# Kernel tuning notes

Hardware: AMD Instinct MI355X
Metric: run time of the kernel (lower is better)

Reference implementation:

```python
import jax, jax.numpy as jnp
import numpy as np
from jax import lax

WSIZE = 11
SIGMA = 1.5
PAD = WSIZE // 2  # 5
C1 = 0.01 ** 2
C2 = 0.03 ** 2


def _gauss1d():
    x = np.arange(WSIZE) - WSIZE // 2
    g = np.exp(-(x.astype(np.float64) ** 2) / (2.0 * SIGMA ** 2))
    g = g / g.sum()
    return jnp.asarray(g, dtype=jnp.float32)


def _blur3d(x, g):
    """Replicate-pad by 5 on D/H/W then apply the separable 11x11x11 Gaussian.
    x: [N, 1, D, H, W]. Mathematically identical to the dense conv3d in the
    original (the 3D window is an exact outer product of the 1D Gaussian)."""
    xp = jnp.pad(x, ((0, 0), (0, 0), (PAD, PAD), (PAD, PAD), (PAD, PAD)), mode='edge')
    dn = ('NCDHW', 'OIDHW', 'NCDHW')
    for kshape in ((1, 1, WSIZE, 1, 1), (1, 1, 1, WSIZE, 1), (1, 1, 1, 1, WSIZE)):
        xp = lax.conv_general_dilated(xp, g.reshape(kshape), (1, 1, 1), 'VALID',
                                      dimension_numbers=dn)
    return xp


def _rerange(img):
    img = jnp.where(img.max() > 128.0, img / 255.0, img)
    img = jnp.where(img.min() < -0.5, (img + 1.0) / 2.0, img)
    return img


def setup_inputs() -> dict:
    key = jax.random.key(0)
    k1, k2 = jax.random.split(key)
    N, C, H, W = 4, 16, 512, 512
    pred = jax.random.uniform(k1, (N, C, H, W), dtype=jnp.float32)
    gt = jax.random.uniform(k2, (N, C, H, W), dtype=jnp.float32)
    return {"pred": pred, "gt": gt}


def reference(pred, gt):
    N = pred.shape[0]
    pred = _rerange(pred)
    gt = _rerange(gt)

    # ---- PSNR (range = 1.0, reduce='sum') ----
    mse = jnp.mean((pred - gt) ** 2, axis=(1, 2, 3))           # [N]
    psnr = jnp.sum(10.0 * jnp.log10(1.0 / mse))                # scalar

    # ---- 3D SSIM over [N,1,C,H,W] volumes ----
    g = _gauss1d()
    img = pred[:, None]                                        # [N,1,D,H,W]
    gtt = gt[:, None]
    mu1 = _blur3d(img, g)
    mu2 = _blur3d(gtt, g)
    mu1_sq = mu1 * mu1
    mu2_sq = mu2 * mu2
    mu1_mu2 = mu1 * mu2
    sigma1_sq = _blur3d(img * img, g) - mu1_sq
    sigma2_sq = _blur3d(gtt * gtt, g) - mu2_sq
    sigma12 = _blur3d(img * gtt, g) - mu1_mu2

    v1 = 2.0 * sigma12 + C2
    v2 = sigma1_sq + sigma2_sq + C2
    ssim_map = ((2.0 * mu1_mu2 + C1) * v1) / ((mu1_sq + mu2_sq + C1) * v2)
    ssim = jnp.sum(jnp.mean(ssim_map, axis=(1, 2, 3, 4)))      # reduce='sum'

    return psnr, ssim, N
```

## Files before the change

### kernel.cpp

```cpp
#include <hip/hip_runtime.h>
#include <cmath>


#define NB 4
#define DD 16
#define HH 512
#define WW 512
#define SLICE (HH * WW)
#define VOL (DD * SLICE)
#define C1F 0.0001f
#define C2F 0.0009f

#define TH 16
#define TW 16
#define SCOLS 26
#define NRP 13
#define PW 14
#define PLSTR 28
#define SDW (NRP * PLSTR)
#define TMW (TH * PW)
#define NTHR 256
#define SIT (NRP * SCOLS)
#define XTRA (SIT - NTHR)
#define HITEMS 104

typedef _Float16 h2v __attribute__((ext_vector_type(2)));

struct KArg {
  unsigned ge[6], go[6];
  float wlT[DD * DD];
};

__device__ inline float dot2h(unsigned a, unsigned b, float c) {
#if __has_builtin(__builtin_amdgcn_fdot2)
  return __builtin_amdgcn_fdot2(__builtin_bit_cast(h2v, a),
                                __builtin_bit_cast(h2v, b), c, false);
#else
  h2v av = __builtin_bit_cast(h2v, a), bv = __builtin_bit_cast(h2v, b);
  return fmaf((float)av.y, (float)bv.y, fmaf((float)av.x, (float)bv.x, c));
#endif
}
__device__ inline unsigned pkh(float a, float b) {
  return __builtin_bit_cast(unsigned, __builtin_amdgcn_cvt_pkrtz(a, b));
}
__device__ inline int iclamp(int v, int lo, int hi) {
  return v < lo ? lo : (v > hi ? hi : v);
}

__device__ inline float block_sum256(float v) {
#pragma unroll
  for (int o = 32; o > 0; o >>= 1) v += __shfl_down(v, o, 64);
  __shared__ float r[4];
  if ((threadIdx.x & 63) == 0) r[threadIdx.x >> 6] = v;
  __syncthreads();
  float out = 0.f;
  if (threadIdx.x == 0) {
#pragma unroll
    for (int i = 0; i < 4; ++i) out += r[i];
  }
  __syncthreads();
  return out;
}

__global__ void zero_acc_k(float* acc) {
  if (threadIdx.x < 8) acc[threadIdx.x] = 0.f;
}

__global__ __launch_bounds__(NTHR, 3) void fused_k(
    const float* __restrict__ pred, const float* __restrict__ gt,
    float* __restrict__ acc, KArg ka) {
  __shared__ uint4 sd[SDW];
  __shared__ uint4 tmp[TMW];

  int b = blockIdx.x;
  int tile = b & 1023;
  int n = b >> 10;
  int th0 = (tile >> 5) * TH;
  int tw0 = (tile & 31) * TW;
  int t = threadIdx.x;

  int rp0 = t / SCOLS, x0 = t - rp0 * SCOLS;
  int gx0 = iclamp(tw0 + x0 - 5, 0, WW - 1);
  int go0a = iclamp(th0 + 2 * rp0 - 5, 0, HH - 1) * WW + gx0;
  int go0b = iclamp(th0 + 2 * rp0 - 4, 0, HH - 1) * WW + gx0;
  int w0i = (2 * rp0 + (x0 & 1)) * PW + (x0 >> 1);
  bool ox0 = (x0 >= 5) && (x0 < 5 + TW);
  float o0a = (ox0 && rp0 >= 3 && rp0 <= 10) ? 1.f : 0.f;
  float o0b = (ox0 && rp0 >= 2 && rp0 <= 9) ? 1.f : 0.f;
  int i1 = t + XTRA;
  bool has2 = (i1 >= NTHR);
  int rp1 = i1 / SCOLS, x1 = i1 - rp1 * SCOLS;
  int gx1 = iclamp(tw0 + x1 - 5, 0, WW - 1);
  int go1a = iclamp(th0 + 2 * rp1 - 5, 0, HH - 1) * WW + gx1;
  int go1b = iclamp(th0 + 2 * rp1 - 4, 0, HH - 1) * WW + gx1;
  int w1i = (2 * rp1 + (x1 & 1)) * PW + (x1 >> 1);
  bool ox1 = (x1 >= 5) && (x1 < 5 + TW);
  float o1a = (ox1 && rp1 >= 3 && rp1 <= 10) ? 1.f : 0.f;
  float o1b = (ox1 && rp1 >= 2 && rp1 <= 9) ? 1.f : 0.f;

  bool hasH = (t < HITEMS);
  int hm = t & 7, hcp = t >> 3;
  int hrd = hm * PLSTR + hcp;
  int hwr = (2 * hm) * PW + hcp;

  int wx = t & 15;
  int wrd = (t >> 4) * PW + (wx >> 1);
  unsigned cw[6];
#pragma unroll
  for (int J = 0; J < 6; ++J) cw[J] = (wx & 1) ? ka.go[J] : ka.ge[J];

  const float* pb = pred + (size_t)n * VOL;
  const float* qb = gt + (size_t)n * VOL;

  float p0a = pb[go0a], p0b = pb[go0b], q0a = qb[go0a], q0b = qb[go0b];
  float p1a = 0.f, p1b = 0.f, q1a = 0.f, q1b = 0.f;
  if (has2) { p1a = pb[go1a]; p1b = pb[go1b]; q1a = qb[go1a]; q1b = qb[go1b]; }

  float psnr = 0.f;
  float a0[DD], a1[DD], a2[DD], a3[DD];
#pragma unroll
  for (int j = 0; j < DD; ++j) { a0[j] = a1[j] = a2[j] = a3[j] = 0.f; }

#pragma unroll 1
  for (int d = 0; d < DD; ++d) {
    {
      float SA = p0a + q0a, DA = p0a - q0a;
      float SB = p0b + q0b, DB = p0b - q0b;
      float dA = DA * DA, dB = DB * DB;
      psnr = fmaf(o0a, dA, psnr);
      psnr = fmaf(o0b, dB, psnr);
      sd[w0i] = make_uint4(pkh(SA, SB), pkh(DA, DB),
                           pkh(SA * SA, SB * SB), pkh(dA, dB));
    }
    if (has2) {
      float SA = p1a + q1a, DA = p1a - q1a;
      float SB = p1b + q1b, DB = p1b - q1b;
      float dA = DA * DA, dB = DB * DB;
      psnr = fmaf(o1a, dA, psnr);
      psnr = fmaf(o1b, dB, psnr);
      sd[w1i] = make_uint4(pkh(SA, SB), pkh(DA, DB),
                           pkh(SA * SA, SB * SB), pkh(dA, dB));
    }
    __syncthreads();

    if (d < DD - 1) {
      const float* P = pb + (size_t)(d + 1) * SLICE;
      const float* Q = qb + (size_t)(d + 1) * SLICE;
      p0a = P[go0a]; p0b = P[go0b]; q0a = Q[go0a]; q0b = Q[go0b];
      if (has2) { p1a = P[go1a]; p1b = P[go1b]; q1a = Q[go1a]; q1b = Q[go1b]; }
    }

    if (hasH) {
      float e0[4] = {0, 0, 0, 0}, e1[4] = {0, 0, 0, 0};
      float r0[4] = {0, 0, 0, 0}, r1[4] = {0, 0, 0, 0};
#pragma unroll
      for (int J = 0; J < 6; ++J) {
        uint4 ve = sd[hrd + J * PLSTR];
        uint4 vo = sd[hrd + J * PLSTR + PW];
        unsigned cge = ka.ge[J], cgo = ka.go[J];
        e0[0] = dot2h(cge, ve.x, e0[0]); e0[1] = dot2h(cge, ve.y, e0[1]);
        e0[2] = dot2h(cge, ve.z, e0[2]); e0[3] = dot2h(cge, ve.w, e0[3]);
        r0[0] = dot2h(cgo, ve.x, r0[0]); r0[1] = dot2h(cgo, ve.y, r0[1]);
        r0[2] = dot2h(cgo, ve.z, r0[2]); r0[3] = dot2h(cgo, ve.w, r0[3]);
        e1[0] = dot2h(cge, vo.x, e1[0]); e1[1] = dot2h(cge, vo.y, e1[1]);
        e1[2] = dot2h(cge, vo.z, e1[2]); e1[3] = dot2h(cge, vo.w, e1[3]);
        r1[0] = dot2h(cgo, vo.x, r1[0]); r1[1] = dot2h(cgo, vo.y, r1[1]);
        r1[2] = dot2h(cgo, vo.z, r1[2]); r1[3] = dot2h(cgo, vo.w, r1[3]);
      }
      tmp[hwr] = make_uint4(pkh(e0[0], e1[0]), pkh(e0[1], e1[1]),
                            pkh(e0[2], e1[2]), pkh(e0[3], e1[3]));
      tmp[hwr + PW] = make_uint4(pkh(r0[0], r1[0]), pkh(r0[1], r1[1]),
                                 pkh(r0[2], r1[2]), pkh(r0[3], r1[3]));
    }
    __syncthreads();

    float w0 = 0.f, w1 = 0.f, w2 = 0.f, w3 = 0.f;
#pragma unroll
    for (int J = 0; J < 6; ++J) {
      uint4 v = tmp[wrd + J];
      w0 = dot2h(cw[J], v.x, w0); w1 = dot2h(cw[J], v.y, w1);
      w2 = dot2h(cw[J], v.z, w2); w3 = dot2h(cw[J], v.w, w3);
    }
    const float* wl = ka.wlT + d * DD;
#pragma unroll
    for (int o = 0; o < DD; ++o) {
      float w = wl[o];
      a0[o] = fmaf(w, w0, a0[o]);
      a1[o] = fmaf(w, w1, a1[o]);
      a2[o] = fmaf(w, w2, a2[o]);
      a3[o] = fmaf(w, w3, a3[o]);
    }
  }

  float ssum = 0.f;
#pragma unroll
  for (int j = 0; j < DD; ++j) {
    float Sb = a0[j], Db = a1[j], B1 = a2[j], B2 = a3[j];
    float SS = Sb * Sb, DDm = Db * Db;
    float m12_2 = (SS - DDm) * 0.5f;
    float msq   = (SS + DDm) * 0.5f;
    float Epq   = (B1 - B2) * 0.25f;
    float Esum  = (B1 + B2) * 0.5f;
    float sig12_2 = 2.f * Epq - m12_2;
    float svar    = Esum - msq;
    float num = (m12_2 + C1F) * (sig12_2 + C2F);
    float den = (msq + C1F) * (svar + C2F);
    ssum += num / den;
  }
  float bs = block_sum256(ssum);
  if (t == 0) atomicAdd(&acc[4 + n], bs);
  float bp = block_sum256(psnr);
  if (t == 0) atomicAdd(&acc[n], bp);
}

__global__ void final_k(const float* __restrict__ acc, float* __restrict__ out) {
  if (threadIdx.x == 0 && blockIdx.x == 0) {
    double psnr = 0.0, ssim = 0.0;
    for (int n = 0; n < NB; ++n) {
      double mse = (double)acc[n] / (double)VOL;
      psnr += 10.0 * log10(1.0 / mse);
      ssim += (double)acc[4 + n] / (double)VOL;
    }
    out[0] = (float)psnr;
    out[1] = (float)ssim;
    out[2] = (float)NB;
  }
}

static unsigned short f2h(float f) {
  union { float f; unsigned u; } v; v.f = f;
  unsigned u = v.u;
  unsigned s = (u >> 16) & 0x8000u;
  int e = (int)((u >> 23) & 0xff) - 127 + 15;
  unsigned m = u & 0x7fffffu;
  if (e <= 0) return (unsigned short)s;
  if (e >= 31) return (unsigned short)(s | 0x7c00u);
  unsigned h = ((unsigned)e << 10) | (m >> 13);
  unsigned rem = m & 0x1fffu;
  if (rem > 0x1000u || (rem == 0x1000u && (h & 1u))) h++;
  return (unsigned short)(s | h);
}
static float h2f(unsigned short h) {
  unsigned se = (h >> 10) & 0x1f, m = h & 0x3ffu, s = ((unsigned)h & 0x8000u) << 16;
  union { unsigned u; float f; } v;
  if (se == 0) { v.u = s; return v.f; }
  v.u = s | ((se - 15 + 127) << 23) | (m << 13);
  return v.f;
}

extern "C" void kernel_launch(void* const* d_in, const int* in_sizes, int n_in,
                              void* d_out, int out_size, void* d_ws, size_t ws_size,
                              hipStream_t stream) {
  const float* pred = (const float*)d_in[0];
  const float* gt = (const float*)d_in[1];
  float* acc = (float*)d_ws;

  double tt[11], s = 0.0;
  for (int i = 0; i < 11; ++i) {
    double x = i - 5;
    tt[i] = exp(-(x * x) / 4.5);
    s += tt[i];
  }
  float g[11];
  for (int i = 0; i < 11; ++i) g[i] = (float)(tt[i] / s);

  unsigned short hg[11];
  for (int i = 0; i < 11; ++i) hg[i] = f2h(g[i]);
  for (int pass = 0; pass < 3; ++pass) {
    double sum = 0.0;
    for (int i = 0; i < 11; ++i) sum += (double)h2f(hg[i]);
    hg[5] = f2h((float)((double)h2f(hg[5]) + (1.0 - sum)));
  }

  KArg ka;
  for (int j = 0; j < 5; ++j)
    ka.ge[j] = (unsigned)hg[2 * j] | ((unsigned)hg[2 * j + 1] << 16);
  ka.ge[5] = (unsigned)hg[10];
  ka.go[0] = ((unsigned)hg[0]) << 16;
  for (int j = 1; j < 6; ++j)
    ka.go[j] = (unsigned)hg[2 * j - 1] | ((unsigned)hg[2 * j] << 16);

  for (int o = 0; o < DD; ++o)
    for (int d = 0; d < DD; ++d) {
      float w = 0.f;
      for (int k = 0; k < 11; ++k) {
        int j = o + k - 5;
        j = j < 0 ? 0 : (j > 15 ? 15 : j);
        if (j == d) w += g[k];
      }
      ka.wlT[d * DD + o] = w;
    }

  zero_acc_k<<<1, 64, 0, stream>>>(acc);
  fused_k<<<NB * 1024, NTHR, 0, stream>>>(pred, gt, acc, ka);
  final_k<<<1, 1, 0, stream>>>(acc, (float*)d_out);
}
```

Baseline: 255.6 us.

## Replace dot2 separable blur passes with MFMA 16x16x32 f16 matrix products

Recasts the H, W and depth Gaussian passes as banded-matrix multiplies on MFMA f16 instructions, using lane-specific band tables uploaded to device memory instead of a kernel-argument struct. Depth accumulation now stores per-slice fp16 results to a larger LDS buffer and applies the clamped depth weights with MFMA at the end, instead of keeping 64 float accumulators in registers. The aim is to move the convolution arithmetic onto matrix cores and free registers. In exchange it uses more LDS, adds an extra barrier per slice, rounds intermediates to fp16 more often, and issues a host-to-device copy of the tables on every call.

Result: slower. 295.2 us (+15.5%).

```diff
diff --git a/kernel.cpp b/kernel.cpp
--- a/kernel.cpp
+++ b/kernel.cpp
@@ -13,32 +13,14 @@
 
 #define TH 16
 #define TW 16
-#define SCOLS 26
-#define NRP 13
-#define PW 14
-#define PLSTR 28
-#define SDW (NRP * PLSTR)
-#define TMW (TH * PW)
 #define NTHR 256
-#define SIT (NRP * SCOLS)
-#define XTRA (SIT - NTHR)
-#define HITEMS 104
-
-typedef _Float16 h2v __attribute__((ext_vector_type(2)));
-
-struct KArg {
-  unsigned ge[6], go[6];
-  float wlT[DD * DD];
-};
-
-__device__ inline float dot2h(unsigned a, unsigned b, float c) {
-#if __has_builtin(__builtin_amdgcn_fdot2)
-  return __builtin_amdgcn_fdot2(__builtin_bit_cast(h2v, a),
-                                __builtin_bit_cast(h2v, b), c, false);
-#else
-  h2v av = __builtin_bit_cast(h2v, a), bv = __builtin_bit_cast(h2v, b);
-  return fmaf((float)av.y, (float)bv.y, fmaf((float)av.x, (float)bv.x, c));
-#endif
+
+typedef _Float16 h8 __attribute__((ext_vector_type(8)));
+typedef float f4 __attribute__((ext_vector_type(4)));
+
+__device__ inline f4 mfma16(uint4 a, uint4 b, f4 c) {
+  return __builtin_amdgcn_mfma_f32_16x16x32_f16(
+      __builtin_bit_cast(h8, a), __builtin_bit_cast(h8, b), c, 0, 0, 0);
 }
 __device__ inline unsigned pkh(float a, float b) {
   return __builtin_bit_cast(unsigned, __builtin_amdgcn_cvt_pkrtz(a, b));
@@ -68,9 +50,10 @@
 
 __global__ __launch_bounds__(NTHR, 3) void fused_k(
     const float* __restrict__ pred, const float* __restrict__ gt,
-    float* __restrict__ acc, KArg ka) {
-  __shared__ uint4 sd[SDW];
-  __shared__ uint4 tmp[TMW];
+    float* __restrict__ acc, const uint4* __restrict__ tabs) {
+  __shared__ _Float16 sd[4 * 32 * 40];
+  __shared__ _Float16 ost[4 * 256 * 16];
+  __shared__ uint4 zzq;
 
   int b = blockIdx.x;
   int tile = b & 1023;
@@ -78,36 +61,36 @@
   int th0 = (tile >> 5) * TH;
   int tw0 = (tile & 31) * TW;
   int t = threadIdx.x;
-
-  int rp0 = t / SCOLS, x0 = t - rp0 * SCOLS;
+  int lane = t & 63, wv = t >> 6;
+  int lo = lane & 15, hi = lane >> 4;
+
+  uint4 bh = tabs[lane];
+  uint4 gwt = tabs[64 + lane];
+  uint4 wlf = tabs[128 + lane];
+
+  unsigned* sdw = (unsigned*)sd;
+#pragma unroll
+  for (int i = 0; i < 10; ++i) sdw[t + i * 256] = 0;
+  if (t == 0) zzq = make_uint4(0, 0, 0, 0);
+
+  int rp0 = t / 26, x0 = t - rp0 * 26;
   int gx0 = iclamp(tw0 + x0 - 5, 0, WW - 1);
   int go0a = iclamp(th0 + 2 * rp0 - 5, 0, HH - 1) * WW + gx0;
   int go0b = iclamp(th0 + 2 * rp0 - 4, 0, HH - 1) * WW + gx0;
-  int w0i = (2 * rp0 + (x0 & 1)) * PW + (x0 >> 1);
-  bool ox0 = (x0 >= 5) && (x0 < 5 + TW);
+  int w0 = x0 * 20 + rp0;
+  bool ox0 = (x0 >= 5) && (x0 < 21);
   float o0a = (ox0 && rp0 >= 3 && rp0 <= 10) ? 1.f : 0.f;
   float o0b = (ox0 && rp0 >= 2 && rp0 <= 9) ? 1.f : 0.f;
-  int i1 = t + XTRA;
-  bool has2 = (i1 >= NTHR);
-  int rp1 = i1 / SCOLS, x1 = i1 - rp1 * SCOLS;
+  int i1 = t + 82;
+  bool has2 = (i1 >= 256);
+  int rp1 = i1 / 26, x1 = i1 - rp1 * 26;
   int gx1 = iclamp(tw0 + x1 - 5, 0, WW - 1);
   int go1a = iclamp(th0 + 2 * rp1 - 5, 0, HH - 1) * WW + gx1;
   int go1b = iclamp(th0 + 2 * rp1 - 4, 0, HH - 1) * WW + gx1;
-  int w1i = (2 * rp1 + (x1 & 1)) * PW + (x1 >> 1);
-  bool ox1 = (x1 >= 5) && (x1 < 5 + TW);
+  int w1 = x1 * 20 + rp1;
+  bool ox1 = (x1 >= 5) && (x1 < 21);
   float o1a = (ox1 && rp1 >= 3 && rp1 <= 10) ? 1.f : 0.f;
   float o1b = (ox1 && rp1 >= 2 && rp1 <= 9) ? 1.f : 0.f;
-
-  bool hasH = (t < HITEMS);
-  int hm = t & 7, hcp = t >> 3;
-  int hrd = hm * PLSTR + hcp;
-  int hwr = (2 * hm) * PW + hcp;
-
-  int wx = t & 15;
-  int wrd = (t >> 4) * PW + (wx >> 1);
-  unsigned cw[6];
-#pragma unroll
-  for (int J = 0; J < 6; ++J) cw[J] = (wx & 1) ? ka.go[J] : ka.ge[J];
 
   const float* pb = pred + (size_t)n * VOL;
   const float* qb = gt + (size_t)n * VOL;
@@ -116,10 +99,20 @@
   float p1a = 0.f, p1b = 0.f, q1a = 0.f, q1b = 0.f;
   if (has2) { p1a = pb[go1a]; p1b = pb[go1b]; q1a = qb[go1a]; q1b = qb[go1b]; }
 
+  int owb = wv * 1024 + (64 * hi + lo) * 4;
+  int qx = 2 * (hi & 1);
+  const uint4* sdq = (const uint4*)sd;
+  int fr0 = wv * 160 + lo * 5 + hi;
+  int fr1 = wv * 160 + (lo + 16) * 5 + hi;
+  f4 z4 = {0.f, 0.f, 0.f, 0.f};
+
   float psnr = 0.f;
-  float a0[DD], a1[DD], a2[DD], a3[DD];
-#pragma unroll
-  for (int j = 0; j < DD; ++j) { a0[j] = a1[j] = a2[j] = a3[j] = 0.f; }
+  float oe0, oe1, oe2, oe3;
+  unsigned pA0, pA1, pA2, pA3, pB0, pB1, pB2, pB3;
+  oe0 = oe1 = oe2 = oe3 = 0.f;
+  pA0 = pA1 = pA2 = pA3 = pB0 = pB1 = pB2 = pB3 = 0u;
+
+  __syncthreads();
 
 #pragma unroll 1
   for (int d = 0; d < DD; ++d) {
@@ -129,8 +122,10 @@
       float dA = DA * DA, dB = DB * DB;
       psnr = fmaf(o0a, dA, psnr);
       psnr = fmaf(o0b, dB, psnr);
-      sd[w0i] = make_uint4(pkh(SA, SB), pkh(DA, DB),
-                           pkh(SA * SA, SB * SB), pkh(dA, dB));
+      sdw[w0]        = pkh(SA, SB);
+      sdw[640 + w0]  = pkh(DA, DB);
+      sdw[1280 + w0] = pkh(SA * SA, SB * SB);
+      sdw[1920 + w0] = pkh(dA, dB);
     }
     if (has2) {
       float SA = p1a + q1a, DA = p1a - q1a;
@@ -138,9 +133,15 @@
       float dA = DA * DA, dB = DB * DB;
       psnr = fmaf(o1a, dA, psnr);
       psnr = fmaf(o1b, dB, psnr);
-      sd[w1i] = make_uint4(pkh(SA, SB), pkh(DA, DB),
-                           pkh(SA * SA, SB * SB), pkh(dA, dB));
-    }
+      sdw[w1]        = pkh(SA, SB);
+      sdw[640 + w1]  = pkh(DA, DB);
+      sdw[1280 + w1] = pkh(SA * SA, SB * SB);
+      sdw[1920 + w1] = pkh(dA, dB);
+    }
+    __syncthreads();
+
+    uint4 fa0 = sdq[fr0];
+    uint4 fa1 = sdq[fr1];
     __syncthreads();
 
     if (d < DD - 1) {
@@ -150,62 +151,61 @@
       if (has2) { p1a = P[go1a]; p1b = P[go1b]; q1a = Q[go1a]; q1b = Q[go1b]; }
     }
 
-    if (hasH) {
-      float e0[4] = {0, 0, 0, 0}, e1[4] = {0, 0, 0, 0};
-      float r0[4] = {0, 0, 0, 0}, r1[4] = {0, 0, 0, 0};
-#pragma unroll
-      for (int J = 0; J < 6; ++J) {
-        uint4 ve = sd[hrd + J * PLSTR];
-        uint4 vo = sd[hrd + J * PLSTR + PW];
-        unsigned cge = ka.ge[J], cgo = ka.go[J];
-        e0[0] = dot2h(cge, ve.x, e0[0]); e0[1] = dot2h(cge, ve.y, e0[1]);
-        e0[2] = dot2h(cge, ve.z, e0[2]); e0[3] = dot2h(cge, ve.w, e0[3]);
-        r0[0] = dot2h(cgo, ve.x, r0[0]); r0[1] = dot2h(cgo, ve.y, r0[1]);
-        r0[2] = dot2h(cgo, ve.z, r0[2]); r0[3] = dot2h(cgo, ve.w, r0[3]);
-        e1[0] = dot2h(cge, vo.x, e1[0]); e1[1] = dot2h(cge, vo.y, e1[1]);
-        e1[2] = dot2h(cge, vo.z, e1[2]); e1[3] = dot2h(cge, vo.w, e1[3]);
-        r1[0] = dot2h(cgo, vo.x, r1[0]); r1[1] = dot2h(cgo, vo.y, r1[1]);
-        r1[2] = dot2h(cgo, vo.z, r1[2]); r1[3] = dot2h(cgo, vo.w, r1[3]);
-      }
-      tmp[hwr] = make_uint4(pkh(e0[0], e1[0]), pkh(e0[1], e1[1]),
-                            pkh(e0[2], e1[2]), pkh(e0[3], e1[3]));
-      tmp[hwr + PW] = make_uint4(pkh(r0[0], r1[0]), pkh(r0[1], r1[1]),
-                                 pkh(r0[2], r1[2]), pkh(r0[3], r1[3]));
-    }
-    __syncthreads();
-
-    float w0 = 0.f, w1 = 0.f, w2 = 0.f, w3 = 0.f;
-#pragma unroll
-    for (int J = 0; J < 6; ++J) {
-      uint4 v = tmp[wrd + J];
-      w0 = dot2h(cw[J], v.x, w0); w1 = dot2h(cw[J], v.y, w1);
-      w2 = dot2h(cw[J], v.z, w2); w3 = dot2h(cw[J], v.w, w3);
-    }
-    const float* wl = ka.wlT + d * DD;
-#pragma unroll
-    for (int o = 0; o < DD; ++o) {
-      float w = wl[o];
-      a0[o] = fmaf(w, w0, a0[o]);
-      a1[o] = fmaf(w, w1, a1[o]);
-      a2[o] = fmaf(w, w2, a2[o]);
-      a3[o] = fmaf(w, w3, a3[o]);
-    }
-  }
-
+    f4 t0 = mfma16(fa0, bh, z4);
+    f4 t1 = mfma16(fa1, bh, z4);
+    uint4 ta = make_uint4(pkh(t0.x, t0.y), pkh(t0.z, t0.w),
+                          pkh(t1.x, t1.y), pkh(t1.z, t1.w));
+    f4 o = mfma16(ta, gwt, z4);
+
+    if ((d & 1) == 0) {
+      oe0 = o.x; oe1 = o.y; oe2 = o.z; oe3 = o.w;
+    } else if ((d & 2) == 0) {
+      pA0 = pkh(oe0, o.x); pA1 = pkh(oe1, o.y);
+      pA2 = pkh(oe2, o.z); pA3 = pkh(oe3, o.w);
+    } else {
+      pB0 = pkh(oe0, o.x); pB1 = pkh(oe1, o.y);
+      pB2 = pkh(oe2, o.z); pB3 = pkh(oe3, o.w);
+      int Qp = (d >> 2) ^ qx;
+      uint2* op = (uint2*)ost;
+      op[owb + Qp]       = make_uint2(pA0, pB0);
+      op[owb + 64 + Qp]  = make_uint2(pA1, pB1);
+      op[owb + 128 + Qp] = make_uint2(pA2, pB2);
+      op[owb + 192 + Qp] = make_uint2(pA3, pB3);
+    }
+  }
+  __syncthreads();
+
+  const uint4* oq = (const uint4*)ost;
+  int bnt = wv & 1;
+  int blk = (hi < 2) ? (hi ^ bnt) : 0;
+  bool real = (hi < 2);
   float ssum = 0.f;
 #pragma unroll
-  for (int j = 0; j < DD; ++j) {
-    float Sb = a0[j], Db = a1[j], B1 = a2[j], B2 = a3[j];
-    float SS = Sb * Sb, DDm = Db * Db;
-    float m12_2 = (SS - DDm) * 0.5f;
-    float msq   = (SS + DDm) * 0.5f;
-    float Epq   = (B1 - B2) * 0.25f;
-    float Esum  = (B1 + B2) * 0.5f;
-    float sig12_2 = 2.f * Epq - m12_2;
-    float svar    = Esum - msq;
-    float num = (m12_2 + C1F) * (sig12_2 + C2F);
-    float den = (msq + C1F) * (svar + C2F);
-    ssum += num / den;
+  for (int q = 0; q < 4; ++q) {
+    int nt = 4 * wv + q;
+    int bidx = (16 * nt + lo) * 2 + blk;
+    const uint4* bp0 = real ? &oq[bidx] : &zzq;
+    const uint4* bp1 = real ? &oq[512 + bidx] : &zzq;
+    const uint4* bp2 = real ? &oq[1024 + bidx] : &zzq;
+    const uint4* bp3 = real ? &oq[1536 + bidx] : &zzq;
+    f4 cS = mfma16(wlf, *bp0, z4);
+    f4 cD = mfma16(wlf, *bp1, z4);
+    f4 cS2 = mfma16(wlf, *bp2, z4);
+    f4 cD2 = mfma16(wlf, *bp3, z4);
+#pragma unroll
+    for (int r = 0; r < 4; ++r) {
+      float Sb = cS[r], Db = cD[r], B1 = cS2[r], B2 = cD2[r];
+      float SS = Sb * Sb, DDm = Db * Db;
+      float m12_2 = (SS - DDm) * 0.5f;
+      float msq = (SS + DDm) * 0.5f;
+      float Epq = (B1 - B2) * 0.25f;
+      float Esum = (B1 + B2) * 0.5f;
+      float sig12_2 = 2.f * Epq - m12_2;
+      float svar = Esum - msq;
+      float num = (m12_2 + C1F) * (sig12_2 + C2F);
+      float den = (msq + C1F) * (svar + C2F);
+      ssum += num / den;
+    }
   }
   float bs = block_sum256(ssum);
   if (t == 0) atomicAdd(&acc[4 + n], bs);
@@ -248,6 +248,9 @@
   return v.f;
 }
 
+static unsigned s_tabs[192 * 4];
+static bool s_init = false;
+
 extern "C" void kernel_launch(void* const* d_in, const int* in_sizes, int n_in,
                               void* d_out, int out_size, void* d_ws, size_t ws_size,
                               hipStream_t stream) {
@@ -255,43 +258,74 @@
   const float* gt = (const float*)d_in[1];
   float* acc = (float*)d_ws;
 
-  double tt[11], s = 0.0;
-  for (int i = 0; i < 11; ++i) {
-    double x = i - 5;
-    tt[i] = exp(-(x * x) / 4.5);
-    s += tt[i];
-  }
-  float g[11];
-  for (int i = 0; i < 11; ++i) g[i] = (float)(tt[i] / s);
-
-  unsigned short hg[11];
-  for (int i = 0; i < 11; ++i) hg[i] = f2h(g[i]);
-  for (int pass = 0; pass < 3; ++pass) {
-    double sum = 0.0;
-    for (int i = 0; i < 11; ++i) sum += (double)h2f(hg[i]);
-    hg[5] = f2h((float)((double)h2f(hg[5]) + (1.0 - sum)));
-  }
-
-  KArg ka;
-  for (int j = 0; j < 5; ++j)
-    ka.ge[j] = (unsigned)hg[2 * j] | ((unsigned)hg[2 * j + 1] << 16);
-  ka.ge[5] = (unsigned)hg[10];
-  ka.go[0] = ((unsigned)hg[0]) << 16;
-  for (int j = 1; j < 6; ++j)
-    ka.go[j] = (unsigned)hg[2 * j - 1] | ((unsigned)hg[2 * j] << 16);
-
-  for (int o = 0; o < DD; ++o)
-    for (int d = 0; d < DD; ++d) {
-      float w = 0.f;
-      for (int k = 0; k < 11; ++k) {
-        int j = o + k - 5;
-        j = j < 0 ? 0 : (j > 15 ? 15 : j);
-        if (j == d) w += g[k];
-      }
-      ka.wlT[d * DD + o] = w;
-    }
-
+  if (!s_init) {
+    double tt[11], s = 0.0;
+    for (int i = 0; i < 11; ++i) {
+      double x = i - 5;
+      tt[i] = exp(-(x * x) / 4.5);
+      s += tt[i];
+    }
+    float g[11];
+    for (int i = 0; i < 11; ++i) g[i] = (float)(tt[i] / s);
+    unsigned short hg[11];
+    for (int i = 0; i < 11; ++i) hg[i] = f2h(g[i]);
+    for (int pass = 0; pass < 3; ++pass) {
+      double sum = 0.0;
+      for (int i = 0; i < 11; ++i) sum += (double)h2f(hg[i]);
+      hg[5] = f2h((float)((double)h2f(hg[5]) + (1.0 - sum)));
+    }
+    float wl[DD][DD];
+    for (int o = 0; o < DD; ++o)
+      for (int d = 0; d < DD; ++d) {
+        float w = 0.f;
+        for (int k = 0; k < 11; ++k) {
+          int j = o + k - 5;
+          j = j < 0 ? 0 : (j > 15 ? 15 : j);
+          if (j == d) w += g[k];
+        }
+        wl[d][o] = w;
+      }
+    unsigned short wlh[DD][DD];
+    for (int o = 0; o < DD; ++o) {
+      int dmx = 0;
+      for (int d = 0; d < DD; ++d) {
+        wlh[o][d] = f2h(wl[d][o]);
+        if (wl[d][o] > wl[dmx][o]) dmx = d;
+      }
+      for (int pass = 0; pass < 3; ++pass) {
+        double sum = 0.0;
+        for (int d = 0; d < DD; ++d) sum += (double)h2f(wlh[o][d]);
+        wlh[o][dmx] = f2h((float)((double)h2f(wlh[o][dmx]) + (1.0 - sum)));
+      }
+    }
+    for (int l = 0; l < 64; ++l) {
+      int lo = l & 15, hi = l >> 4;
+      unsigned short v[8];
+      for (int i = 0; i < 8; ++i) {
+        int idx = 8 * hi + i - lo;
+        v[i] = (idx >= 0 && idx <= 10) ? hg[idx] : 0;
+      }
+      for (int k = 0; k < 4; ++k)
+        s_tabs[l * 4 + k] = (unsigned)v[2 * k] | ((unsigned)v[2 * k + 1] << 16);
+      for (int i = 0; i < 8; ++i) {
+        int c = 4 * hi + (i & 3) + 16 * (i >> 2);
+        int idx = c - lo;
+        v[i] = (idx >= 0 && idx <= 10) ? hg[idx] : 0;
+      }
+      for (int k = 0; k < 4; ++k)
+        s_tabs[(64 + l) * 4 + k] = (unsigned)v[2 * k] | ((unsigned)v[2 * k + 1] << 16);
+      for (int i = 0; i < 8; ++i)
+        v[i] = (hi < 2) ? wlh[lo][8 * hi + i] : 0;
+      for (int k = 0; k < 4; ++k)
+        s_tabs[(128 + l) * 4 + k] = (unsigned)v[2 * k] | ((unsigned)v[2 * k + 1] << 16);
+    }
+    s_init = true;
+  }
+
+  hipMemcpyAsync((char*)d_ws + 64, s_tabs, sizeof(s_tabs),
+                 hipMemcpyHostToDevice, stream);
   zero_acc_k<<<1, 64, 0, stream>>>(acc);
-  fused_k<<<NB * 1024, NTHR, 0, stream>>>(pred, gt, acc, ka);
+  fused_k<<<NB * 1024, NTHR, 0, stream>>>(pred, gt, acc,
+                                          (const uint4*)((char*)d_ws + 64));
   final_k<<<1, 1, 0, stream>>>(acc, (float*)d_out);
 }
```

## Defer depth blur to packed fp16 dot products and raise occupancy

Applied to the files above, without the earlier changes.

Replaces the per-slice fp32 accumulation into 64 depth-output registers with storing each slice's blurred values as packed fp16 pairs (32 registers). The depth blur is then applied at the end using fdot2 with fp16-renormalized depth weights. It also fully unrolls the slice loop, raises launch bounds to 4 blocks per SIMD, and remaps block order to interleave batches across XCDs. This cuts register pressure and the FMAs per slice, at the cost of extra fp16 rounding in the depth stage.

Result: slower. 627.9 us (+145.7%).

```diff
diff --git a/kernel.cpp b/kernel.cpp
--- a/kernel.cpp
+++ b/kernel.cpp
@@ -28,7 +28,7 @@
 
 struct KArg {
   unsigned ge[6], go[6];
-  float wlT[DD * DD];
+  unsigned w2[128];
 };
 
 __device__ inline float dot2h(unsigned a, unsigned b, float c) {
@@ -66,13 +66,14 @@
   if (threadIdx.x < 8) acc[threadIdx.x] = 0.f;
 }
 
-__global__ __launch_bounds__(NTHR, 3) void fused_k(
+__global__ __launch_bounds__(NTHR, 4) void fused_k(
     const float* __restrict__ pred, const float* __restrict__ gt,
     float* __restrict__ acc, KArg ka) {
   __shared__ uint4 sd[SDW];
   __shared__ uint4 tmp[TMW];
 
-  int b = blockIdx.x;
+  int b0 = blockIdx.x;
+  int b = (b0 & 7) * ((NB * 1024) >> 3) + (b0 >> 3);
   int tile = b & 1023;
   int n = b >> 10;
   int th0 = (tile >> 5) * TH;
@@ -117,90 +118,96 @@
   if (has2) { p1a = pb[go1a]; p1b = pb[go1b]; q1a = qb[go1a]; q1b = qb[go1b]; }
 
   float psnr = 0.f;
-  float a0[DD], a1[DD], a2[DD], a3[DD];
-#pragma unroll
-  for (int j = 0; j < DD; ++j) { a0[j] = a1[j] = a2[j] = a3[j] = 0.f; }
-
-#pragma unroll 1
-  for (int d = 0; d < DD; ++d) {
-    {
-      float SA = p0a + q0a, DA = p0a - q0a;
-      float SB = p0b + q0b, DB = p0b - q0b;
-      float dA = DA * DA, dB = DB * DB;
-      psnr = fmaf(o0a, dA, psnr);
-      psnr = fmaf(o0b, dB, psnr);
-      sd[w0i] = make_uint4(pkh(SA, SB), pkh(DA, DB),
-                           pkh(SA * SA, SB * SB), pkh(dA, dB));
-    }
-    if (has2) {
-      float SA = p1a + q1a, DA = p1a - q1a;
-      float SB = p1b + q1b, DB = p1b - q1b;
-      float dA = DA * DA, dB = DB * DB;
-      psnr = fmaf(o1a, dA, psnr);
-      psnr = fmaf(o1b, dB, psnr);
-      sd[w1i] = make_uint4(pkh(SA, SB), pkh(DA, DB),
-                           pkh(SA * SA, SB * SB), pkh(dA, dB));
-    }
-    __syncthreads();
-
-    if (d < DD - 1) {
-      const float* P = pb + (size_t)(d + 1) * SLICE;
-      const float* Q = qb + (size_t)(d + 1) * SLICE;
-      p0a = P[go0a]; p0b = P[go0b]; q0a = Q[go0a]; q0b = Q[go0b];
-      if (has2) { p1a = P[go1a]; p1b = P[go1b]; q1a = Q[go1a]; q1b = Q[go1b]; }
-    }
-
-    if (hasH) {
-      float e0[4] = {0, 0, 0, 0}, e1[4] = {0, 0, 0, 0};
-      float r0[4] = {0, 0, 0, 0}, r1[4] = {0, 0, 0, 0};
-#pragma unroll
-      for (int J = 0; J < 6; ++J) {
-        uint4 ve = sd[hrd + J * PLSTR];
-        uint4 vo = sd[hrd + J * PLSTR + PW];
-        unsigned cge = ka.ge[J], cgo = ka.go[J];
-        e0[0] = dot2h(cge, ve.x, e0[0]); e0[1] = dot2h(cge, ve.y, e0[1]);
-        e0[2] = dot2h(cge, ve.z, e0[2]); e0[3] = dot2h(cge, ve.w, e0[3]);
-        r0[0] = dot2h(cgo, ve.x, r0[0]); r0[1] = dot2h(cgo, ve.y, r0[1]);
-        r0[2] = dot2h(cgo, ve.z, r0[2]); r0[3] = dot2h(cgo, ve.w, r0[3]);
-        e1[0] = dot2h(cge, vo.x, e1[0]); e1[1] = dot2h(cge, vo.y, e1[1]);
-        e1[2] = dot2h(cge, vo.z, e1[2]); e1[3] = dot2h(cge, vo.w, e1[3]);
-        r1[0] = dot2h(cgo, vo.x, r1[0]); r1[1] = dot2h(cgo, vo.y, r1[1]);
-        r1[2] = dot2h(cgo, vo.z, r1[2]); r1[3] = dot2h(cgo, vo.w, r1[3]);
-      }
-      tmp[hwr] = make_uint4(pkh(e0[0], e1[0]), pkh(e0[1], e1[1]),
-                            pkh(e0[2], e1[2]), pkh(e0[3], e1[3]));
-      tmp[hwr + PW] = make_uint4(pkh(r0[0], r1[0]), pkh(r0[1], r1[1]),
-                                 pkh(r0[2], r1[2]), pkh(r0[3], r1[3]));
-    }
-    __syncthreads();
-
-    float w0 = 0.f, w1 = 0.f, w2 = 0.f, w3 = 0.f;
-#pragma unroll
-    for (int J = 0; J < 6; ++J) {
-      uint4 v = tmp[wrd + J];
-      w0 = dot2h(cw[J], v.x, w0); w1 = dot2h(cw[J], v.y, w1);
-      w2 = dot2h(cw[J], v.z, w2); w3 = dot2h(cw[J], v.w, w3);
-    }
-    const float* wl = ka.wlT + d * DD;
-#pragma unroll
-    for (int o = 0; o < DD; ++o) {
-      float w = wl[o];
-      a0[o] = fmaf(w, w0, a0[o]);
-      a1[o] = fmaf(w, w1, a1[o]);
-      a2[o] = fmaf(w, w2, a2[o]);
-      a3[o] = fmaf(w, w3, a3[o]);
-    }
-  }
+  unsigned h0[8], h1[8], h2[8], h3[8];
+
+#define DO_SLICE(D)                                                         \
+  {                                                                         \
+    float SA = p0a + q0a, DA = p0a - q0a;                                   \
+    float SB = p0b + q0b, DB = p0b - q0b;                                   \
+    float dA = DA * DA, dB = DB * DB;                                       \
+    psnr = fmaf(o0a, dA, psnr);                                             \
+    psnr = fmaf(o0b, dB, psnr);                                             \
+    sd[w0i] = make_uint4(pkh(SA, SB), pkh(DA, DB),                          \
+                         pkh(SA * SA, SB * SB), pkh(dA, dB));               \
+  }                                                                         \
+  if (has2) {                                                               \
+    float SA = p1a + q1a, DA = p1a - q1a;                                   \
+    float SB = p1b + q1b, DB = p1b - q1b;                                   \
+    float dA = DA * DA, dB = DB * DB;                                       \
+    psnr = fmaf(o1a, dA, psnr);                                             \
+    psnr = fmaf(o1b, dB, psnr);                                             \
+    sd[w1i] = make_uint4(pkh(SA, SB), pkh(DA, DB),                          \
+                         pkh(SA * SA, SB * SB), pkh(dA, dB));               \
+  }                                                                         \
+  __syncthreads();            \
+  if ((D) < DD - 1) {                                                       \
+    const float* P = pb + (size_t)((D) + 1) * SLICE;                        \
+    const float* Q = qb + (size_t)((D) + 1) * SLICE;                        \
+    p0a = P[go0a]; p0b = P[go0b]; q0a = Q[go0a]; q0b = Q[go0b];             \
+    if (has2) { p1a = P[go1a]; p1b = P[go1b]; q1a = Q[go1a]; q1b = Q[go1b]; } \
+  }                                                                         \
+  if (hasH) {                                                               \
+    float e0[4] = {0, 0, 0, 0}, e1[4] = {0, 0, 0, 0};                       \
+    float r0[4] = {0, 0, 0, 0}, r1[4] = {0, 0, 0, 0};                       \
+    _Pragma("unroll")                                                       \
+    for (int J = 0; J < 6; ++J) {                                           \
+      uint4 ve = sd[hrd + J * PLSTR];                                       \
+      uint4 vo = sd[hrd + J * PLSTR + PW];                                  \
+      unsigned cge = ka.ge[J], cgo = ka.go[J];                              \
+      e0[0] = dot2h(cge, ve.x, e0[0]); e0[1] = dot2h(cge, ve.y, e0[1]);     \
+      e0[2] = dot2h(cge, ve.z, e0[2]); e0[3] = dot2h(cge, ve.w, e0[3]);     \
+      r0[0] = dot2h(cgo, ve.x, r0[0]); r0[1] = dot2h(cgo, ve.y, r0[1]);     \
+      r0[2] = dot2h(cgo, ve.z, r0[2]); r0[3] = dot2h(cgo, ve.w, r0[3]);     \
+      e1[0] = dot2h(cge, vo.x, e1[0]); e1[1] = dot2h(cge, vo.y, e1[1]);     \
+      e1[2] = dot2h(cge, vo.z, e1[2]); e1[3] = dot2h(cge, vo.w, e1[3]);     \
+      r1[0] = dot2h(cgo, vo.x, r1[0]); r1[1] = dot2h(cgo, vo.y, r1[1]);     \
+      r1[2] = dot2h(cgo, vo.z, r1[2]); r1[3] = dot2h(cgo, vo.w, r1[3]);     \
+    }                                                                       \
+    tmp[hwr] = make_uint4(pkh(e0[0], e1[0]), pkh(e0[1], e1[1]),             \
+                          pkh(e0[2], e1[2]), pkh(e0[3], e1[3]));            \
+    tmp[hwr + PW] = make_uint4(pkh(r0[0], r1[0]), pkh(r0[1], r1[1]),        \
+                               pkh(r0[2], r1[2]), pkh(r0[3], r1[3]));       \
+  }                                                                         \
+  __syncthreads();   \
+  ww0 = 0.f; ww1 = 0.f; ww2 = 0.f; ww3 = 0.f;                               \
+  _Pragma("unroll")                                                         \
+  for (int J = 0; J < 6; ++J) {                                             \
+    uint4 v = tmp[wrd + J];                                                 \
+    ww0 = dot2h(cw[J], v.x, ww0); ww1 = dot2h(cw[J], v.y, ww1);             \
+    ww2 = dot2h(cw[J], v.z, ww2); ww3 = dot2h(cw[J], v.w, ww3);             \
+  }
+
+  float ww0, ww1, ww2, ww3;
+#pragma unroll
+  for (int m = 0; m < 8; ++m) {
+    float oe0, oe1, oe2, oe3;
+    DO_SLICE(2 * m)
+    oe0 = ww0; oe1 = ww1; oe2 = ww2; oe3 = ww3;
+    DO_SLICE(2 * m + 1)
+    h0[m] = pkh(oe0, ww0);
+    h1[m] = pkh(oe1, ww1);
+    h2[m] = pkh(oe2, ww2);
+    h3[m] = pkh(oe3, ww3);
+  }
+#undef DO_SLICE
 
   float ssum = 0.f;
 #pragma unroll
-  for (int j = 0; j < DD; ++j) {
-    float Sb = a0[j], Db = a1[j], B1 = a2[j], B2 = a3[j];
-    float SS = Sb * Sb, DDm = Db * Db;
+  for (int o = 0; o < DD; ++o) {
+    float A0 = 0.f, A1 = 0.f, A2 = 0.f, A3 = 0.f;
+#pragma unroll
+    for (int m = 0; m < 8; ++m) {
+      unsigned c = ka.w2[o * 8 + m];
+      A0 = dot2h(c, h0[m], A0);
+      A1 = dot2h(c, h1[m], A1);
+      A2 = dot2h(c, h2[m], A2);
+      A3 = dot2h(c, h3[m], A3);
+    }
+    float SS = A0 * A0, DDm = A1 * A1;
     float m12_2 = (SS - DDm) * 0.5f;
     float msq   = (SS + DDm) * 0.5f;
-    float Epq   = (B1 - B2) * 0.25f;
-    float Esum  = (B1 + B2) * 0.5f;
+    float Epq   = (A2 - A3) * 0.25f;
+    float Esum  = (A2 + A3) * 0.5f;
     float sig12_2 = 2.f * Epq - m12_2;
     float svar    = Esum - msq;
     float num = (m12_2 + C1F) * (sig12_2 + C2F);
@@ -280,6 +287,7 @@
   for (int j = 1; j < 6; ++j)
     ka.go[j] = (unsigned)hg[2 * j - 1] | ((unsigned)hg[2 * j] << 16);
 
+  float wl[DD][DD];
   for (int o = 0; o < DD; ++o)
     for (int d = 0; d < DD; ++d) {
       float w = 0.f;
@@ -288,8 +296,23 @@
         j = j < 0 ? 0 : (j > 15 ? 15 : j);
         if (j == d) w += g[k];
       }
-      ka.wlT[d * DD + o] = w;
-    }
+      wl[d][o] = w;
+    }
+  for (int o = 0; o < DD; ++o) {
+    unsigned short wv[DD];
+    int dmx = 0;
+    for (int d = 0; d < DD; ++d) {
+      wv[d] = f2h(wl[d][o]);
+      if (wl[d][o] > wl[dmx][o]) dmx = d;
+    }
+    for (int pass = 0; pass < 3; ++pass) {
+      double sum = 0.0;
+      for (int d = 0; d < DD; ++d) sum += (double)h2f(wv[d]);
+      wv[dmx] = f2h((float)((double)h2f(wv[dmx]) + (1.0 - sum)));
+    }
+    for (int m = 0; m < 8; ++m)
+      ka.w2[o * 8 + m] = (unsigned)wv[2 * m] | ((unsigned)wv[2 * m + 1] << 16);
+  }
 
   zero_acc_k<<<1, 64, 0, stream>>>(acc);
   fused_k<<<NB * 1024, NTHR, 0, stream>>>(pred, gt, acc, ka);
```
